# Performance work log

Measured on AMD Instinct MI355X. Metric: run time of the kernel, lower is better.

Reference implementation:

```python
import jax, jax.numpy as jnp
import numpy as np

N, B, T, H, M, DM, K = 256, 32, 128, 64, 8, 32, 3
IN_DIM = 1
OUT_DIM = 1
DEC_H = H + DM  # 96


def _p(key, shape):
    return jax.random.normal(key, shape, jnp.float32) / np.sqrt(shape[0]).astype(np.float32)


def setup_inputs() -> dict:
    key = jax.random.key(0)
    ks = jax.random.split(key, 10)
    gdi = 2 * K * (IN_DIM + H)      # 390
    ddi = 2 * K * (OUT_DIM + DEC_H)  # 582
    return {
        'x': jax.random.normal(ks[0], (B, T, N, IN_DIM), jnp.float32),
        'Memory': _p(ks[1], (M, DM)),
        'Wq': _p(ks[2], (H, DM)),
        'We1': _p(ks[3], (N, M)),
        'We2': _p(ks[4], (N, M)),
        'enc_gate_w': _p(ks[5], (gdi, 2 * H)), 'enc_gate_b': jnp.zeros((2 * H,), jnp.float32),
        'enc_upd_w': _p(ks[6], (gdi, H)), 'enc_upd_b': jnp.zeros((H,), jnp.float32),
        'dec_gate_w': _p(ks[7], (ddi, 2 * DEC_H)), 'dec_gate_b': jnp.zeros((2 * DEC_H,), jnp.float32),
        'dec_upd_w': _p(ks[8], (ddi, DEC_H)), 'dec_upd_b': jnp.zeros((DEC_H,), jnp.float32),
        'proj_w': _p(ks[9], (DEC_H, OUT_DIM)), 'proj_b': jnp.zeros((OUT_DIM,), jnp.float32),
    }


def _cheb(s):
    # Chebyshev polynomials T_0..T_{K-1} of support s: [I, s, 2 s T_{k-1} - T_{k-2}]
    polys = [jnp.eye(N, dtype=s.dtype), s]
    for _ in range(2, K):
        polys.append(2.0 * s @ polys[-1] - polys[-2])
    return polys


def _scaled_lap(e1, e2, gkey):
    # cosine-similarity graph -> straight-through gumbel hard selection -> scaled Laplacian
    norm = jnp.linalg.norm(e1, axis=1, keepdims=True) @ jnp.linalg.norm(e2, axis=1, keepdims=True).T
    g = (e1 @ e2.T) / (norm + 1e-6)
    g = (g + 1.0) / 2.0
    logits = jnp.stack([g, 1.0 - g], axis=-1)               # (N,N,2)
    y_soft = logits + jax.random.gumbel(gkey, logits.shape, logits.dtype)  # tau=1 (note: source skips softmax)
    y_hard = jax.nn.one_hot(jnp.argmax(y_soft, axis=-1), 2, dtype=logits.dtype)
    adj = (y_hard - jax.lax.stop_gradient(y_soft) + y_soft)[:, :, 0]
    eye = jnp.eye(N, dtype=adj.dtype)
    adj = adj * (1.0 - eye)                                  # zero diagonal
    d = jnp.sum(adj, axis=1)
    L = jnp.diag(d) - adj
    lam = L.max() - L.min()
    return 2.0 * L / lam - eye


def _gconv(x, S, w, b):
    # S: (2K,N,N) stacked cheb supports; x: (B,N,C)
    xg = jnp.einsum('knm,bmc->bnkc', S, x)
    xg = xg.reshape(xg.shape[0], xg.shape[1], -1)            # (B,N,2K*C), support-major like torch cat
    return xg @ w + b


def _cell(x, state, S, gw, gb, uw, ub, hid):
    zr = jax.nn.sigmoid(_gconv(jnp.concatenate([x, state], -1), S, gw, gb))
    z, r = zr[..., :hid], zr[..., hid:]
    hc = jnp.tanh(_gconv(jnp.concatenate([x, z * state], -1), S, uw, ub))
    return r * state + (1.0 - r) * hc


def reference(x, Memory, Wq, We1, We2, enc_gate_w, enc_gate_b, enc_upd_w, enc_upd_b,
              dec_gate_w, dec_gate_b, dec_upd_w, dec_upd_b, proj_w, proj_b):
    k1, k2 = jax.random.split(jax.random.key(42))
    e1, e2 = We1 @ Memory, We2 @ Memory
    S = jnp.stack(_cheb(_scaled_lap(e1, e2, k1)) + _cheb(_scaled_lap(e2, e1, k2)))  # (2K,N,N)

    # --- encoder (1 layer) over time ---
    def enc_step(state, xt):
        h = _cell(xt, state, S, enc_gate_w, enc_gate_b, enc_upd_w, enc_upd_b, H)
        return h, None
    h0 = jnp.zeros((x.shape[0], N, H), x.dtype)
    h_t, _ = jax.lax.scan(enc_step, h0, jnp.swapaxes(x, 0, 1))

    # --- memory attention query ---
    query = h_t @ Wq                                        # (B,N,DM)
    att = jax.nn.softmax(query @ Memory.T, axis=-1)         # (B,N,M)
    value = att @ Memory                                    # (B,N,DM)
    h_de = jnp.concatenate([h_t, value], -1)                # (B,N,DEC_H)

    go0 = jnp.zeros((x.shape[0], N, OUT_DIM), x.dtype)
    def dec_step(carry, _):
        state, go = carry
        h = _cell(go, state, S, dec_gate_w, dec_gate_b, dec_upd_w, dec_upd_b, DEC_H)
        go = h @ proj_w + proj_b
        return (h, go), go
    _, outs = jax.lax.scan(dec_step, (h_de, go0), None, length=T)
    return jnp.swapaxes(outs, 0, 1)                         # (B,T,N,OUT_DIM)
```

## Files before the change

### kernel.cpp

```cpp
#include <hip/hip_runtime.h>
#include <stdint.h>
#include <math.h>

#define NNODE 256
#define BATCH 32
#define TLEN  128
#define ROWS  8192

typedef unsigned short u16;
typedef short bf16x8 __attribute__((ext_vector_type(8)));
typedef float f32x4 __attribute__((ext_vector_type(4)));

__device__ inline u16 f2bf_rn(float v) {
  uint32_t u = __float_as_uint(v);
  u += 0x7fffu + ((u >> 16) & 1u);
  return (u16)(u >> 16);
}
__device__ inline float bf2f(u16 h) { return __uint_as_float(((uint32_t)h) << 16); }
__device__ inline void split2(float v, u16& hi, u16& lo) {
  hi = f2bf_rn(v);
  lo = f2bf_rn(v - bf2f(hi));
}

__device__ inline size_t pk_addr(int c, int b, int n) {
  return ((((size_t)(c >> 4) * 32 + b) * 8 + (n >> 5)) << 9) +
         (((size_t)((c & 15) | (((n >> 3) & 3) << 4))) << 3) + (n & 7);
}

__host__ __device__ inline uint32_t rotl32_(uint32_t v, int d) {
  return (v << d) | (v >> (32 - d));
}
__host__ __device__ inline void tf2x32(uint32_t k0, uint32_t k1, uint32_t x0,
                                       uint32_t x1, uint32_t* o0, uint32_t* o1) {
  uint32_t ks2 = k0 ^ k1 ^ 0x1BD11BDAu;
  x0 += k0; x1 += k1;
  x0 += x1; x1 = rotl32_(x1, 13); x1 ^= x0;
  x0 += x1; x1 = rotl32_(x1, 15); x1 ^= x0;
  x0 += x1; x1 = rotl32_(x1, 26); x1 ^= x0;
  x0 += x1; x1 = rotl32_(x1, 6);  x1 ^= x0;
  x0 += k1; x1 += ks2 + 1u;
  x0 += x1; x1 = rotl32_(x1, 17); x1 ^= x0;
  x0 += x1; x1 = rotl32_(x1, 29); x1 ^= x0;
  x0 += x1; x1 = rotl32_(x1, 16); x1 ^= x0;
  x0 += x1; x1 = rotl32_(x1, 24); x1 ^= x0;
  x0 += ks2; x1 += k0 + 2u;
  x0 += x1; x1 = rotl32_(x1, 13); x1 ^= x0;
  x0 += x1; x1 = rotl32_(x1, 15); x1 ^= x0;
  x0 += x1; x1 = rotl32_(x1, 26); x1 ^= x0;
  x0 += x1; x1 = rotl32_(x1, 6);  x1 ^= x0;
  x0 += k0; x1 += k1 + 3u;
  x0 += x1; x1 = rotl32_(x1, 17); x1 ^= x0;
  x0 += x1; x1 = rotl32_(x1, 29); x1 ^= x0;
  x0 += x1; x1 = rotl32_(x1, 16); x1 ^= x0;
  x0 += x1; x1 = rotl32_(x1, 24); x1 ^= x0;
  x0 += k1; x1 += ks2 + 4u;
  x0 += x1; x1 = rotl32_(x1, 13); x1 ^= x0;
  x0 += x1; x1 = rotl32_(x1, 15); x1 ^= x0;
  x0 += x1; x1 = rotl32_(x1, 26); x1 ^= x0;
  x0 += x1; x1 = rotl32_(x1, 6);  x1 ^= x0;
  x0 += ks2; x1 += k0 + 5u;
  *o0 = x0; *o1 = x1;
}

__device__ inline float gumbel_at(uint32_t k0, uint32_t k1, uint32_t idx) {
  uint32_t o0, o1;
  tf2x32(k0, k1, 0u, idx, &o0, &o1);
  uint32_t b = o0 ^ o1;
  float f = __uint_as_float((b >> 9) | 0x3f800000u) - 1.0f;
  const float tiny = 1.17549435e-38f;
  float u = fmaxf(tiny, f + tiny);
  return -logf(-logf(u));
}

__global__ __launch_bounds__(256) void setup_embed_kernel(
    const float* __restrict__ We1, const float* __restrict__ We2,
    const float* __restrict__ Mem, float* __restrict__ e1, float* __restrict__ e2,
    float* __restrict__ n1, float* __restrict__ n2) {
  int n = threadIdx.x;
  float a[8];
  float s;
  for (int m = 0; m < 8; ++m) a[m] = We1[n * 8 + m];
  s = 0.f;
  for (int j = 0; j < 32; ++j) {
    float v = 0.f;
    for (int m = 0; m < 8; ++m) v = fmaf(a[m], Mem[m * 32 + j], v);
    e1[n * 32 + j] = v;
    s = fmaf(v, v, s);
  }
  n1[n] = sqrtf(s);
  for (int m = 0; m < 8; ++m) a[m] = We2[n * 8 + m];
  s = 0.f;
  for (int j = 0; j < 32; ++j) {
    float v = 0.f;
    for (int m = 0; m < 8; ++m) v = fmaf(a[m], Mem[m * 32 + j], v);
    e2[n * 32 + j] = v;
    s = fmaf(v, v, s);
  }
  n2[n] = sqrtf(s);
}

__global__ void stats_init_kernel(int* stats) {
  stats[0] = 0;
  stats[1] = 0;
  stats[2] = 0x7fffffff;
}

__global__ __launch_bounds__(256) void adj_kernel(
    const float* __restrict__ eA, const float* __restrict__ eB,
    const float* __restrict__ nA, const float* __restrict__ nB,
    uint32_t k0, uint32_t k1, float* __restrict__ adj, float* __restrict__ deg,
    int* __restrict__ stats) {
  int i = blockIdx.x, j = threadIdx.x;
  float dot = 0.f;
  for (int c = 0; c < 32; ++c) dot = fmaf(eA[i * 32 + c], eB[j * 32 + c], dot);
  float g = dot / (nA[i] * nB[j] + 1e-6f);
  g = (g + 1.0f) * 0.5f;
  uint32_t f = ((uint32_t)(i * 256 + j)) * 2u;
  float g0 = gumbel_at(k0, k1, f);
  float g1 = gumbel_at(k0, k1, f + 1u);
  float a = ((g + g0) >= ((1.0f - g) + g1)) ? 1.0f : 0.0f;
  if (i == j) a = 0.0f;
  adj[i * 256 + j] = a;
  __shared__ float red[256];
  red[j] = a;
  __syncthreads();
  for (int s = 128; s > 0; s >>= 1) {
    if (j < s) red[j] += red[j + s];
    __syncthreads();
  }
  if (j == 0) {
    float d = red[0];
    deg[i] = d;
    atomicMax(&stats[0], (int)d);
    atomicMin(&stats[2], (int)d);
    if (d > 0.5f) atomicOr(&stats[1], 1);
  }
}

__global__ __launch_bounds__(256) void lap_kernel(const float* __restrict__ adj,
                                                  const float* __restrict__ deg,
                                                  const int* __restrict__ stats,
                                                  float* __restrict__ S1) {
  int i = blockIdx.x, j = threadIdx.x;
  float lmax = (float)stats[0];
  float lmin = stats[1] ? -1.0f : (float)stats[2];
  float lam = lmax - lmin;
  float L = (i == j) ? deg[i] : -adj[i * 256 + j];
  S1[i * 256 + j] = 2.0f * L / lam - ((i == j) ? 1.0f : 0.0f);
}

__global__ __launch_bounds__(256) void t2_kernel(const float* __restrict__ A,
                                                 float* __restrict__ Cout) {
  __shared__ __align__(16) float sAT[32][68];
  __shared__ __align__(16) float sB[32][68];
  int tid = threadIdx.x;
  int tc = tid & 15, tr = tid >> 4;
  int row0 = blockIdx.y * 64, col0 = blockIdx.x * 64;
  float acc[4][4] = {};
  for (int m0 = 0; m0 < 256; m0 += 32) {
    for (int i = tid; i < 2048; i += 256) {
      int r = i >> 5, c = i & 31;
      sAT[c][r] = A[(size_t)(row0 + r) * 256 + m0 + c];
    }
    for (int i = tid; i < 2048; i += 256) {
      int r = i >> 6, c = i & 63;
      sB[r][c] = A[(size_t)(m0 + r) * 256 + col0 + c];
    }
    __syncthreads();
#pragma unroll
    for (int kk = 0; kk < 32; ++kk) {
      float4 av = *(const float4*)&sAT[kk][tr * 4];
      float4 bv = *(const float4*)&sB[kk][tc * 4];
      float a[4] = {av.x, av.y, av.z, av.w};
      float b[4] = {bv.x, bv.y, bv.z, bv.w};
#pragma unroll
      for (int i = 0; i < 4; ++i)
#pragma unroll
        for (int j = 0; j < 4; ++j) acc[i][j] = fmaf(a[i], b[j], acc[i][j]);
    }
    __syncthreads();
  }
#pragma unroll
  for (int i = 0; i < 4; ++i) {
    int row = row0 + tr * 4 + i;
#pragma unroll
    for (int j = 0; j < 4; ++j) {
      int col = col0 + tc * 4 + j;
      Cout[(size_t)row * 256 + col] = 2.0f * acc[i][j] - ((row == col) ? 1.0f : 0.0f);
    }
  }
}

__global__ void cvt_s_packed(const float* __restrict__ S, u16* __restrict__ Sh,
                             u16* __restrict__ Sl) {
  int idx = blockIdx.x * 256 + threadIdx.x;
  if (idx >= 4 * 65536) return;
  int p = idx >> 16, rem = idx & 65535;
  int n = rem >> 8, m = rem & 255;
  int nt = n >> 4, li = n & 15;
  int mc = m >> 5, g = (m >> 3) & 3, j = m & 7;
  int lane = li | (g << 4);
  size_t a = (((size_t)(p * 16 + nt) * 8 + mc) << 9) + lane * 8 + j;
  u16 h, l;
  split2(S[idx], h, l);
  Sh[a] = h; Sl[a] = l;
}

__global__ void build_wfrag(const float* __restrict__ W, int C, int O, int hid,
                            u16* __restrict__ WfH, u16* __restrict__ WfL,
                            float* __restrict__ w0, float* __restrict__ wlast) {
  int idx = blockIdx.x * 256 + threadIdx.x;
  int nKC = hid / 32;
  if (idx < 5 * hid * O) {
    int kk = idx & 31;
    int rest = idx >> 5;
    int o = rest % O; rest /= O;
    int kc = rest % nKC;
    int p = rest / nKC;
    int korig = (p == 0) ? 0 : (p + (p >= 3 ? 1 : 0));
    int c = kc * 32 + kk;
    float v = 0.f;
    if (c > 0) {
      v = W[(size_t)(korig * C + c) * O + o];
      if (p == 0) v += W[(size_t)(3 * C + c) * O + o];
    }
    int ot = o >> 4, li = o & 15, g = kk >> 3, j = kk & 7;
    int lane = li | (g << 4);
    size_t a = (((size_t)(p * nKC + kc) * (O / 16) + ot) << 9) + lane * 8 + j;
    u16 h, l; split2(v, h, l);
    WfH[a] = h; WfL[a] = l;
  }
  if (idx < 5 * O) {
    int o = idx % O, p = idx / O;
    int korig = (p == 0) ? 0 : (p + (p >= 3 ? 1 : 0));
    float v0 = W[(size_t)(korig * C + 0) * O + o];
    if (p == 0) v0 += W[(size_t)(3 * C + 0) * O + o];
    w0[p * O + o] = v0;
    float vl = W[(size_t)(korig * C + hid) * O + o];
    if (p == 0) vl += W[(size_t)(3 * C + hid) * O + o];
    wlast[p * O + o] = vl;
  }
}

__global__ void zero_kernel(uint4* __restrict__ p, int n4) {
  for (int i = blockIdx.x * blockDim.x + threadIdx.x; i < n4;
       i += gridDim.x * blockDim.x)
    p[i] = make_uint4(0, 0, 0, 0);
}

__global__ void enc_init(const float* __restrict__ x,
                         u16* __restrict__ pkh, u16* __restrict__ pkl) {
  int col = blockIdx.x * 256 + threadIdx.x;
  if (col >= ROWS) return;
  int b = col >> 8, n = col & 255;
  float v = x[(size_t)b * (TLEN * NNODE) + n];
  u16 h, l; split2(v, h, l);
  size_t a = pk_addr(0, b, n);
  pkh[a] = h; pkl[a] = l;
}

__global__ __launch_bounds__(128) void attn2(const u16* __restrict__ hEh,
                                             const u16* __restrict__ hEl,
                                             const float* __restrict__ Wq,
                                             const float* __restrict__ Mem,
                                             u16* __restrict__ pkh,
                                             u16* __restrict__ pkl) {
  int col = blockIdx.x * 128 + threadIdx.x;
  int b = col >> 8, n = col & 255;
  float h[64];
  for (int c = 0; c < 64; ++c) {
    size_t a = pk_addr(1 + c, b, n);
    h[c] = bf2f(hEh[a]) + bf2f(hEl[a]);
  }
  float q[32];
  for (int j = 0; j < 32; ++j) {
    float s = 0.f;
    for (int c = 0; c < 64; ++c) s = fmaf(h[c], Wq[c * 32 + j], s);
    q[j] = s;
  }
  float l[8], mx = -3.402823466e38f;
  for (int m = 0; m < 8; ++m) {
    float s = 0.f;
    for (int j = 0; j < 32; ++j) s = fmaf(q[j], Mem[m * 32 + j], s);
    l[m] = s;
    mx = fmaxf(mx, s);
  }
  float se = 0.f;
  for (int m = 0; m < 8; ++m) { l[m] = expf(l[m] - mx); se += l[m]; }
  float val[32];
  for (int j = 0; j < 32; ++j) {
    float v = 0.f;
    for (int m = 0; m < 8; ++m) v = fmaf(l[m] / se, Mem[m * 32 + j], v);
    val[j] = v;
  }
  for (int c = 0; c < 97; ++c) {
    float v = (c == 0) ? 0.f : ((c <= 64) ? h[c - 1] : val[c - 65]);
    u16 hh, ll; split2(v, hh, ll);
    size_t a = pk_addr(c, b, n);
    pkh[a] = hh; pkl[a] = ll;
  }
}

template <int C, int HID, int O, int NKC, int MT1, int MODE>
__global__ __launch_bounds__(1024, 4) void fused_step(
    const u16* __restrict__ ApkH, const u16* __restrict__ ApkL,
    const u16* __restrict__ SpkH, const u16* __restrict__ SpkL,
    const u16* __restrict__ WpkH, const u16* __restrict__ WpkL,
    const float* __restrict__ w0, const float* __restrict__ wlast,
    const float* __restrict__ bias,
    const u16* __restrict__ stH, const u16* __restrict__ stL,
    u16* __restrict__ outPkH, u16* __restrict__ outPkL,
    float* __restrict__ rbuf,
    const float* __restrict__ xsrc, int tnext,
    const float* __restrict__ pw, const float* __restrict__ pb,
    float* __restrict__ outp, int tcur) {
  constexpr int MT2 = O / 16;
  constexpr int MT1A = (MT1 + 1) / 2;
  constexpr int CH0SLOT = HID + 1;
  constexpr int KS8 = (HID + 9) / 8;

  __shared__ __align__(16) u16 GhR[(size_t)2 * 5 * KS8 * 16 * 8];
  __shared__ __align__(16) u16 GlR[(size_t)2 * 5 * KS8 * 16 * 8];
  __shared__ float projL[(MODE == 2) ? 32 * 100 : 4];

  auto Gidx = [](int c2, int p, int li, int slot) -> size_t {
    return (((size_t)((c2 * 5 + p) * KS8 + (slot >> 3)) * 16 + li) << 3) +
           (slot & 7);
  };

  const int tid = threadIdx.x;
  const int wid = tid >> 6, lane = tid & 63;
  const int g = lane >> 4, li = lane & 15;
  const int cgi = wid >> 3, pp = wid & 3, half = (wid >> 2) & 1;
  const int bid0 = (int)blockIdx.x;
  const int bidx = ((bid0 & 7) << 5) | (bid0 >> 3);
  const int col0 = bidx * 32;
  const int b = col0 >> 8;
  const int nb = col0 & 255;
  const int n0 = nb + cgi * 16;
  const int nt = n0 >> 4;

  for (int i = tid; i < 32 * C; i += 1024) {
    int c = i >> 5, q = i & 31;
    size_t a = pk_addr(c, b, nb + q);
    int slot = (c == 0) ? CH0SLOT : c;
    GhR[Gidx(q >> 4, 0, q & 15, slot)] = ApkH[a];
    GlR[Gidx(q >> 4, 0, q & 15, slot)] = ApkL[a];
  }
  if (tid < 32) {
    GhR[Gidx(tid >> 4, 0, tid & 15, 0)] = 0;
    GlR[Gidx(tid >> 4, 0, tid & 15, 0)] = 0;
  }

  f32x4 acc1[MT1A];
#pragma unroll
  for (int i = 0; i < MT1A; ++i) acc1[i] = (f32x4){0.f, 0.f, 0.f, 0.f};

#pragma unroll 2
  for (int mc = 0; mc < 8; ++mc) {
    size_t sa = (((size_t)(pp * 16 + nt) * 8 + mc) << 9) + lane * 8;
    bf16x8 sbh = *(const bf16x8*)(SpkH + sa);
    bf16x8 sbl = *(const bf16x8*)(SpkL + sa);
#pragma unroll
    for (int i = 0; i < MT1A; ++i) {
      const int mt = half * MT1A + i;
      if (mt < MT1) {
        size_t aa = (((size_t)(mt * 32 + b) * 8 + mc) << 9) + lane * 8;
        bf16x8 ah = *(const bf16x8*)(ApkH + aa);
        bf16x8 al = *(const bf16x8*)(ApkL + aa);
        acc1[i] = __builtin_amdgcn_mfma_f32_16x16x32_bf16(ah, sbh, acc1[i], 0, 0, 0);
        acc1[i] = __builtin_amdgcn_mfma_f32_16x16x32_bf16(ah, sbl, acc1[i], 0, 0, 0);
        acc1[i] = __builtin_amdgcn_mfma_f32_16x16x32_bf16(al, sbh, acc1[i], 0, 0, 0);
      }
    }
  }

  {
    const int p = pp + 1;
#pragma unroll
    for (int i = 0; i < MT1A; ++i) {
      const int mt = half * MT1A + i;
      if (mt < MT1) {
        int cq = mt * 16 + 4 * g;
        u16 h4[4], l4[4];
#pragma unroll
        for (int r = 0; r < 4; ++r) split2(acc1[i][r], h4[r], l4[r]);
        if (cq == 0) {
          GhR[Gidx(cgi, p, li, CH0SLOT)] = h4[0];
          GlR[Gidx(cgi, p, li, CH0SLOT)] = l4[0];
          h4[0] = 0; l4[0] = 0;
        }
        if (cq + 3 <= HID) {
          uint2 vh, vl;
          vh.x = (uint32_t)h4[0] | ((uint32_t)h4[1] << 16);
          vh.y = (uint32_t)h4[2] | ((uint32_t)h4[3] << 16);
          vl.x = (uint32_t)l4[0] | ((uint32_t)l4[1] << 16);
          vl.y = (uint32_t)l4[2] | ((uint32_t)l4[3] << 16);
          *(uint2*)&GhR[Gidx(cgi, p, li, cq)] = vh;
          *(uint2*)&GlR[Gidx(cgi, p, li, cq)] = vl;
        } else {
#pragma unroll
          for (int r = 0; r < 4; ++r) {
            int c = cq + r;
            if (c >= 1 && c <= HID) {
              GhR[Gidx(cgi, p, li, c)] = h4[r];
              GlR[Gidx(cgi, p, li, c)] = l4[r];
            }
          }
        }
      }
    }
  }
  __syncthreads();

  const int mt2 = wid;
  f32x4 acc2[2];
  acc2[0] = (f32x4){0.f, 0.f, 0.f, 0.f};
  acc2[1] = (f32x4){0.f, 0.f, 0.f, 0.f};
  if (mt2 < MT2) {
#pragma unroll
    for (int p = 0; p < 5; ++p) {
#pragma unroll
      for (int kc = 0; kc < NKC; ++kc) {
        bf16x8 bh[2], bl[2];
#pragma unroll
        for (int c2 = 0; c2 < 2; ++c2) {
          bh[c2] = *(const bf16x8*)&GhR[Gidx(c2, p, li, kc * 32 + g * 8)];
          bl[c2] = *(const bf16x8*)&GlR[Gidx(c2, p, li, kc * 32 + g * 8)];
        }
        size_t wa = (((size_t)(p * NKC + kc) * MT2 + mt2) << 9) + lane * 8;
        bf16x8 wh = *(const bf16x8*)(WpkH + wa);
        bf16x8 wl = *(const bf16x8*)(WpkL + wa);
#pragma unroll
        for (int c2 = 0; c2 < 2; ++c2) {
          acc2[c2] = __builtin_amdgcn_mfma_f32_16x16x32_bf16(wh, bh[c2], acc2[c2], 0, 0, 0);
          acc2[c2] = __builtin_amdgcn_mfma_f32_16x16x32_bf16(wh, bl[c2], acc2[c2], 0, 0, 0);
          acc2[c2] = __builtin_amdgcn_mfma_f32_16x16x32_bf16(wl, bh[c2], acc2[c2], 0, 0, 0);
        }
      }
    }
  }

  float ch0v[2][5], clv[2][5];
#pragma unroll
  for (int c2 = 0; c2 < 2; ++c2)
#pragma unroll
    for (int p = 0; p < 5; ++p) {
      if (p == 0) {
        size_t a = pk_addr(0, b, nb + c2 * 16 + li);
        ch0v[c2][p] = bf2f(ApkH[a]) + bf2f(ApkL[a]);
      } else {
        ch0v[c2][p] = bf2f(GhR[Gidx(c2, p, li, CH0SLOT)]) +
                      bf2f(GlR[Gidx(c2, p, li, CH0SLOT)]);
      }
      clv[c2][p] = bf2f(GhR[Gidx(c2, p, li, HID)]) + bf2f(GlR[Gidx(c2, p, li, HID)]);
    }

  if (mt2 < MT2) {
#pragma unroll
    for (int c2 = 0; c2 < 2; ++c2) {
      const int ncolx = nb + c2 * 16 + li;
      const int colx = col0 + c2 * 16 + li;
#pragma unroll
      for (int r = 0; r < 4; ++r) {
        int o = mt2 * 16 + 4 * g + r;
        float v = acc2[c2][r] + bias[o];
#pragma unroll
        for (int p = 0; p < 5; ++p) {
          v = fmaf(w0[p * O + o], ch0v[c2][p], v);
          v = fmaf(wlast[p * O + o], clv[c2][p], v);
        }
        size_t a = pk_addr(1 + o, b, ncolx);
        if (MODE == 0) {
          float s = 1.0f / (1.0f + expf(-v));
          if (o < HID) {
            float hrec = bf2f(stH[a]) + bf2f(stL[a]);
            float u = s * hrec;
            u16 h_, l_; split2(u, h_, l_);
            outPkH[a] = h_; outPkL[a] = l_;
          } else {
            rbuf[(size_t)(o - HID) * ROWS + colx] = s;
          }
        } else {
          float hc = tanhf(v);
          float hp = bf2f(stH[a]) + bf2f(stL[a]);
          float rr = rbuf[(size_t)o * ROWS + colx];
          float hn = rr * hp + (1.0f - rr) * hc;
          u16 h_, l_; split2(hn, h_, l_);
          outPkH[a] = h_; outPkL[a] = l_;
          if (MODE == 2) projL[((size_t)c2 * 16 + li) * 100 + o] = hn;
        }
      }
    }
  }

  if (MODE == 0) {
    if (tid < 32) {
      size_t a = pk_addr(0, b, nb + tid);
      outPkH[a] = ApkH[a];
      outPkL[a] = ApkL[a];
    }
  }
  if (MODE == 1) {
    if (tnext >= 0 && tid < 32) {
      int n = nb + tid;
      float xv = xsrc[(size_t)b * (TLEN * NNODE) + (size_t)tnext * NNODE + n];
      u16 h_, l_; split2(xv, h_, l_);
      size_t a = pk_addr(0, b, n);
      outPkH[a] = h_; outPkL[a] = l_;
    }
  }
  if (MODE == 2) {
    __syncthreads();
    if (tid < 32) {
      int n = nb + tid;
      float s = pb[0];
#pragma unroll
      for (int o = 0; o < HID; ++o) s = fmaf(pw[o], projL[(size_t)tid * 100 + o], s);
      u16 h_, l_; split2(s, h_, l_);
      size_t a = pk_addr(0, b, n);
      outPkH[a] = h_; outPkL[a] = l_;
      outp[((size_t)b * TLEN + tcur) * NNODE + n] = s;
    }
  }
}

extern "C" void kernel_launch(void* const* d_in, const int* in_sizes, int n_in,
                              void* d_out, int out_size, void* d_ws, size_t ws_size,
                              hipStream_t stream) {
  (void)in_sizes; (void)n_in; (void)out_size; (void)ws_size;
  const float* x   = (const float*)d_in[0];
  const float* Mem = (const float*)d_in[1];
  const float* Wq  = (const float*)d_in[2];
  const float* We1 = (const float*)d_in[3];
  const float* We2 = (const float*)d_in[4];
  const float* egw = (const float*)d_in[5];
  const float* egb = (const float*)d_in[6];
  const float* euw = (const float*)d_in[7];
  const float* eub = (const float*)d_in[8];
  const float* dgw = (const float*)d_in[9];
  const float* dgb = (const float*)d_in[10];
  const float* duw = (const float*)d_in[11];
  const float* dub = (const float*)d_in[12];
  const float* pw  = (const float*)d_in[13];
  const float* pb  = (const float*)d_in[14];
  float* out = (float*)d_out;

  float* ws = (float*)d_ws;
  size_t off = 0;
  auto allocf = [&](size_t nf) {
    float* p = ws + off;
    off += (nf + 63) & ~(size_t)63;
    return p;
  };
  auto allocu = [&](size_t nu) { return (u16*)allocf((nu + 1) / 2); };

  float* Sf  = allocf(4 * 65536);
  float* e1  = allocf(8192);
  float* e2  = allocf(8192);
  float* n1  = allocf(256);
  float* n2  = allocf(256);
  float* adj = allocf(65536);
  float* deg = allocf(256);
  int* stats = (int*)allocf(64);
  float* rb  = allocf((size_t)96 * ROWS);
  float* w0gE = allocf(5 * 128);
  float* w0uE = allocf(5 * 64);
  float* w0gD = allocf(5 * 192);
  float* w0uD = allocf(5 * 96);
  float* wlgE = allocf(5 * 128);
  float* wluE = allocf(5 * 64);
  float* wlgD = allocf(5 * 192);
  float* wluD = allocf(5 * 96);

  u16* SpkH = allocu((size_t)4 * 65536);
  u16* SpkL = allocu((size_t)4 * 65536);
  u16* WgEh = allocu((size_t)5 * 2 * 8 * 512);
  u16* WgEl = allocu((size_t)5 * 2 * 8 * 512);
  u16* WuEh = allocu((size_t)5 * 2 * 4 * 512);
  u16* WuEl = allocu((size_t)5 * 2 * 4 * 512);
  u16* WgDh = allocu((size_t)5 * 3 * 12 * 512);
  u16* WgDl = allocu((size_t)5 * 3 * 12 * 512);
  u16* WuDh = allocu((size_t)5 * 3 * 6 * 512);
  u16* WuDl = allocu((size_t)5 * 3 * 6 * 512);

  const size_t PKE = (size_t)5 * 32 * 8 * 512;
  const size_t PKD = (size_t)7 * 32 * 8 * 512;
  u16* hEpkH = allocu(PKE);
  u16* hEpkL = allocu(PKE);
  u16* uEpkH = allocu(PKE);
  u16* uEpkL = allocu(PKE);
  u16* hDpkH = allocu(PKD);
  u16* hDpkL = allocu(PKD);
  u16* uDpkH = allocu(PKD);
  u16* uDpkL = allocu(PKD);
  const size_t PKTOT = 4 * PKE + 4 * PKD;

  uint32_t ka0, ka1, kb0, kb1;
  tf2x32(0u, 42u, 0u, 0u, &ka0, &ka1);
  tf2x32(0u, 42u, 0u, 1u, &kb0, &kb1);

  zero_kernel<<<1024, 256, 0, stream>>>((uint4*)hEpkH, (int)(PKTOT / 8));
  setup_embed_kernel<<<1, 256, 0, stream>>>(We1, We2, Mem, e1, e2, n1, n2);
  stats_init_kernel<<<1, 1, 0, stream>>>(stats);
  adj_kernel<<<256, 256, 0, stream>>>(e1, e2, n1, n2, ka0, ka1, adj, deg, stats);
  lap_kernel<<<256, 256, 0, stream>>>(adj, deg, stats, Sf);
  t2_kernel<<<dim3(4, 4), 256, 0, stream>>>(Sf, Sf + 65536);
  stats_init_kernel<<<1, 1, 0, stream>>>(stats);
  adj_kernel<<<256, 256, 0, stream>>>(e2, e1, n2, n1, kb0, kb1, adj, deg, stats);
  lap_kernel<<<256, 256, 0, stream>>>(adj, deg, stats, Sf + 2 * 65536);
  t2_kernel<<<dim3(4, 4), 256, 0, stream>>>(Sf + 2 * 65536, Sf + 3 * 65536);
  cvt_s_packed<<<1024, 256, 0, stream>>>(Sf, SpkH, SpkL);
  build_wfrag<<<(5 * 64 * 128 + 255) / 256, 256, 0, stream>>>(egw, 65, 128, 64, WgEh, WgEl, w0gE, wlgE);
  build_wfrag<<<(5 * 64 * 64 + 255) / 256, 256, 0, stream>>>(euw, 65, 64, 64, WuEh, WuEl, w0uE, wluE);
  build_wfrag<<<(5 * 96 * 192 + 255) / 256, 256, 0, stream>>>(dgw, 97, 192, 96, WgDh, WgDl, w0gD, wlgD);
  build_wfrag<<<(5 * 96 * 96 + 255) / 256, 256, 0, stream>>>(duw, 97, 96, 96, WuDh, WuDl, w0uD, wluD);

  enc_init<<<32, 256, 0, stream>>>(x, hEpkH, hEpkL);
  for (int t = 0; t < TLEN; ++t) {
    fused_step<65, 64, 128, 2, 5, 0><<<256, 1024, 0, stream>>>(
        hEpkH, hEpkL, SpkH, SpkL, WgEh, WgEl, w0gE, wlgE, egb,
        hEpkH, hEpkL, uEpkH, uEpkL, rb, nullptr, -1, nullptr, nullptr, nullptr, 0);
    fused_step<65, 64, 64, 2, 5, 1><<<256, 1024, 0, stream>>>(
        uEpkH, uEpkL, SpkH, SpkL, WuEh, WuEl, w0uE, wluE, eub,
        hEpkH, hEpkL, hEpkH, hEpkL, rb,
        x, (t + 1 < TLEN) ? (t + 1) : -1, nullptr, nullptr, nullptr, 0);
  }

  attn2<<<64, 128, 0, stream>>>(hEpkH, hEpkL, Wq, Mem, hDpkH, hDpkL);

  for (int t = 0; t < TLEN; ++t) {
    fused_step<97, 96, 192, 3, 7, 0><<<256, 1024, 0, stream>>>(
        hDpkH, hDpkL, SpkH, SpkL, WgDh, WgDl, w0gD, wlgD, dgb,
        hDpkH, hDpkL, uDpkH, uDpkL, rb, nullptr, -1, nullptr, nullptr, nullptr, 0);
    fused_step<97, 96, 96, 3, 7, 2><<<256, 1024, 0, stream>>>(
        uDpkH, uDpkL, SpkH, SpkL, WuDh, WuDl, w0uD, wluD, dub,
        hDpkH, hDpkL, hDpkH, hDpkL, rb,
        nullptr, -1, pw, pb, out, t);
  }
}
```

Measured before the change: 8.008 ms.

## Replace per-step kernel launches with persistent cooperative kernels using per-XCD barriers

Encoder and decoder time loops now each run inside one cooperative persistent kernel. Half-steps are separated by atomic-counter barriers scoped to groups of 32 blocks (blockIdx & 7), replacing 512 separate kernel launches. The A-operand fragments are also staged once per block into shared memory, using sc0 loads that bypass stale cache lines, instead of each wave reading them from global memory. This cuts launch overhead and redundant global loads but relies on the assumption that each group of 32 blocks only exchanges data within that group. It also keeps the old multi-launch path as a fallback if the cooperative launch fails.

```diff
diff --git a/kernel.cpp b/kernel.cpp
--- a/kernel.cpp
+++ b/kernel.cpp
@@ -25,6 +25,12 @@
 __device__ inline size_t pk_addr(int c, int b, int n) {
   return ((((size_t)(c >> 4) * 32 + b) * 8 + (n >> 5)) << 9) +
          (((size_t)((c & 15) | (((n >> 3) & 3) << 4))) << 3) + (n & 7);
+}
+
+__device__ __forceinline__ bf16x8 load16_sc0(const u16* p) {
+  bf16x8 r;
+  asm volatile("global_load_dwordx4 %0, %1, off sc0" : "=v"(r) : "v"(p));
+  return r;
 }
 
 __host__ __device__ inline uint32_t rotl32_(uint32_t v, int d) {
@@ -302,26 +308,24 @@
 }
 
 template <int C, int HID, int O, int NKC, int MT1, int MODE>
-__global__ __launch_bounds__(1024, 4) void fused_step(
-    const u16* __restrict__ ApkH, const u16* __restrict__ ApkL,
-    const u16* __restrict__ SpkH, const u16* __restrict__ SpkL,
-    const u16* __restrict__ WpkH, const u16* __restrict__ WpkL,
-    const float* __restrict__ w0, const float* __restrict__ wlast,
-    const float* __restrict__ bias,
-    const u16* __restrict__ stH, const u16* __restrict__ stL,
-    u16* __restrict__ outPkH, u16* __restrict__ outPkL,
-    float* __restrict__ rbuf,
-    const float* __restrict__ xsrc, int tnext,
-    const float* __restrict__ pw, const float* __restrict__ pb,
-    float* __restrict__ outp, int tcur) {
+__device__ __forceinline__ void half_step(
+    const u16* ApkH, const u16* ApkL,
+    const u16* SpkH, const u16* SpkL,
+    const u16* WpkH, const u16* WpkL,
+    const float* w0, const float* wlast, const float* bias,
+    const u16* stH, const u16* stL,
+    u16* outPkH, u16* outPkL,
+    float* rbuf, const float* xsrc, int tnext,
+    const float* pw, const float* pb, float* outp, int tcur,
+    u16* GhR, u16* GlR, u16* stg) {
   constexpr int MT2 = O / 16;
   constexpr int MT1A = (MT1 + 1) / 2;
   constexpr int CH0SLOT = HID + 1;
   constexpr int KS8 = (HID + 9) / 8;
-
-  __shared__ __align__(16) u16 GhR[(size_t)2 * 5 * KS8 * 16 * 8];
-  __shared__ __align__(16) u16 GlR[(size_t)2 * 5 * KS8 * 16 * 8];
-  __shared__ float projL[(MODE == 2) ? 32 * 100 : 4];
+  constexpr int NFR = MT1 * 8;
+  constexpr int KTRIP = (NFR + 15) / 16;
+
+  float* projL = (float*)stg;
 
   auto Gidx = [](int c2, int p, int li, int slot) -> size_t {
     return (((size_t)((c2 * 5 + p) * KS8 + (slot >> 3)) * 16 + li) << 3) +
@@ -340,39 +344,65 @@
   const int n0 = nb + cgi * 16;
   const int nt = n0 >> 4;
 
-  for (int i = tid; i < 32 * C; i += 1024) {
-    int c = i >> 5, q = i & 31;
-    size_t a = pk_addr(c, b, nb + q);
-    int slot = (c == 0) ? CH0SLOT : c;
-    GhR[Gidx(q >> 4, 0, q & 15, slot)] = ApkH[a];
-    GlR[Gidx(q >> 4, 0, q & 15, slot)] = ApkL[a];
-  }
-  if (tid < 32) {
-    GhR[Gidx(tid >> 4, 0, tid & 15, 0)] = 0;
-    GlR[Gidx(tid >> 4, 0, tid & 15, 0)] = 0;
-  }
-
   f32x4 acc1[MT1A];
 #pragma unroll
   for (int i = 0; i < MT1A; ++i) acc1[i] = (f32x4){0.f, 0.f, 0.f, 0.f};
 
-#pragma unroll 2
-  for (int mc = 0; mc < 8; ++mc) {
-    size_t sa = (((size_t)(pp * 16 + nt) * 8 + mc) << 9) + lane * 8;
-    bf16x8 sbh = *(const bf16x8*)(SpkH + sa);
-    bf16x8 sbl = *(const bf16x8*)(SpkL + sa);
-#pragma unroll
-    for (int i = 0; i < MT1A; ++i) {
-      const int mt = half * MT1A + i;
-      if (mt < MT1) {
-        size_t aa = (((size_t)(mt * 32 + b) * 8 + mc) << 9) + lane * 8;
-        bf16x8 ah = *(const bf16x8*)(ApkH + aa);
-        bf16x8 al = *(const bf16x8*)(ApkL + aa);
-        acc1[i] = __builtin_amdgcn_mfma_f32_16x16x32_bf16(ah, sbh, acc1[i], 0, 0, 0);
-        acc1[i] = __builtin_amdgcn_mfma_f32_16x16x32_bf16(ah, sbl, acc1[i], 0, 0, 0);
-        acc1[i] = __builtin_amdgcn_mfma_f32_16x16x32_bf16(al, sbh, acc1[i], 0, 0, 0);
-      }
-    }
+#pragma unroll
+  for (int r = 0; r < 2; ++r) {
+    bf16x8 areg[KTRIP];
+#pragma unroll
+    for (int k = 0; k < KTRIP; ++k) {
+      int f = wid + k * 16;
+      if (f < NFR) {
+        int hl = f & 1, rest = f >> 1;
+        int mt = rest % MT1, mcl = rest / MT1;
+        int mc = r * 4 + mcl;
+        const u16* src = (hl ? ApkL : ApkH) +
+                         ((((size_t)(mt * 32 + b) * 8 + mc) << 9) + lane * 8);
+        areg[k] = load16_sc0(src);
+      }
+    }
+    if (r == 0) {
+      for (int i = tid; i < 32 * C; i += 1024) {
+        int c = i >> 5, q = i & 31;
+        size_t a = pk_addr(c, b, nb + q);
+        int slot = (c == 0) ? CH0SLOT : c;
+        GhR[Gidx(q >> 4, 0, q & 15, slot)] = ApkH[a];
+        GlR[Gidx(q >> 4, 0, q & 15, slot)] = ApkL[a];
+      }
+      if (tid < 32) {
+        GhR[Gidx(tid >> 4, 0, tid & 15, 0)] = 0;
+        GlR[Gidx(tid >> 4, 0, tid & 15, 0)] = 0;
+      }
+    }
+    asm volatile("s_waitcnt vmcnt(0)" ::: "memory");
+#pragma unroll
+    for (int k = 0; k < KTRIP; ++k) {
+      int f = wid + k * 16;
+      if (f < NFR) *(bf16x8*)&stg[(size_t)f * 512 + lane * 8] = areg[k];
+    }
+    __syncthreads();
+#pragma unroll
+    for (int mcl = 0; mcl < 4; ++mcl) {
+      int mc = r * 4 + mcl;
+      size_t sa = (((size_t)(pp * 16 + nt) * 8 + mc) << 9) + lane * 8;
+      bf16x8 sbh = *(const bf16x8*)(SpkH + sa);
+      bf16x8 sbl = *(const bf16x8*)(SpkL + sa);
+#pragma unroll
+      for (int i = 0; i < MT1A; ++i) {
+        const int mt = half * MT1A + i;
+        if (mt < MT1) {
+          const size_t fb = (size_t)((mcl * MT1 + mt) * 2) * 512 + lane * 8;
+          bf16x8 ah = *(const bf16x8*)&stg[fb];
+          bf16x8 al = *(const bf16x8*)&stg[fb + 512];
+          acc1[i] = __builtin_amdgcn_mfma_f32_16x16x32_bf16(ah, sbh, acc1[i], 0, 0, 0);
+          acc1[i] = __builtin_amdgcn_mfma_f32_16x16x32_bf16(ah, sbl, acc1[i], 0, 0, 0);
+          acc1[i] = __builtin_amdgcn_mfma_f32_16x16x32_bf16(al, sbh, acc1[i], 0, 0, 0);
+        }
+      }
+    }
+    __syncthreads();
   }
 
   {
@@ -525,6 +555,77 @@
   }
 }
 
+__device__ __forceinline__ void xcd_barrier(int* bar, int grp, int target) {
+  asm volatile("s_waitcnt vmcnt(0)" ::: "memory");
+  __syncthreads();
+  if (threadIdx.x == 0) {
+    __hip_atomic_fetch_add(&bar[grp * 32], 1, __ATOMIC_RELAXED,
+                           __HIP_MEMORY_SCOPE_AGENT);
+    while (__hip_atomic_load(&bar[grp * 32], __ATOMIC_RELAXED,
+                             __HIP_MEMORY_SCOPE_AGENT) < target)
+      __builtin_amdgcn_s_sleep(1);
+  }
+  __syncthreads();
+}
+
+template <int C, int HID, int O, int NKC, int MT1, int MODE>
+__global__ __launch_bounds__(1024, 4) void fused_step(
+    const u16* __restrict__ ApkH, const u16* __restrict__ ApkL,
+    const u16* __restrict__ SpkH, const u16* __restrict__ SpkL,
+    const u16* __restrict__ WpkH, const u16* __restrict__ WpkL,
+    const float* __restrict__ w0, const float* __restrict__ wlast,
+    const float* __restrict__ bias,
+    const u16* __restrict__ stH, const u16* __restrict__ stL,
+    u16* __restrict__ outPkH, u16* __restrict__ outPkL,
+    float* __restrict__ rbuf,
+    const float* __restrict__ xsrc, int tnext,
+    const float* __restrict__ pw, const float* __restrict__ pb,
+    float* __restrict__ outp, int tcur) {
+  constexpr int KS8 = (HID + 9) / 8;
+  __shared__ __align__(16) u16 GhR[(size_t)2 * 5 * KS8 * 16 * 8];
+  __shared__ __align__(16) u16 GlR[(size_t)2 * 5 * KS8 * 16 * 8];
+  __shared__ __align__(16) u16 stg[(size_t)MT1 * 8 * 512];
+  half_step<C, HID, O, NKC, MT1, MODE>(
+      ApkH, ApkL, SpkH, SpkL, WpkH, WpkL, w0, wlast, bias, stH, stL,
+      outPkH, outPkL, rbuf, xsrc, tnext, pw, pb, outp, tcur, GhR, GlR, stg);
+}
+
+struct PhaseP {
+  const float* xsrc;
+  u16 *hPkH, *hPkL, *uPkH, *uPkL;
+  const u16 *SpkH, *SpkL;
+  const u16 *WgH, *WgL; const float *w0g, *wlg, *bg;
+  const u16 *WuH, *WuL; const float *w0u, *wlu, *bu;
+  float* rbuf;
+  const float *pw, *pb; float* outp;
+  int* bar;
+};
+
+template <int C, int HID, int Og, int Ou, int NKC, int MT1, int UPDM>
+__global__ __launch_bounds__(1024, 4) void persistent_phase(PhaseP P) {
+  constexpr int KS8 = (HID + 9) / 8;
+  __shared__ __align__(16) u16 GhR[(size_t)2 * 5 * KS8 * 16 * 8];
+  __shared__ __align__(16) u16 GlR[(size_t)2 * 5 * KS8 * 16 * 8];
+  __shared__ __align__(16) u16 stg[(size_t)MT1 * 8 * 512];
+  const int grp = (int)blockIdx.x & 7;
+  int ep = 0;
+  for (int t = 0; t < TLEN; ++t) {
+    half_step<C, HID, Og, NKC, MT1, 0>(
+        P.hPkH, P.hPkL, P.SpkH, P.SpkL, P.WgH, P.WgL, P.w0g, P.wlg, P.bg,
+        P.hPkH, P.hPkL, P.uPkH, P.uPkL, P.rbuf, nullptr, -1,
+        nullptr, nullptr, nullptr, 0, GhR, GlR, stg);
+    ++ep;
+    xcd_barrier(P.bar, grp, 32 * ep);
+    half_step<C, HID, Ou, NKC, MT1, UPDM>(
+        P.uPkH, P.uPkL, P.SpkH, P.SpkL, P.WuH, P.WuL, P.w0u, P.wlu, P.bu,
+        P.hPkH, P.hPkL, P.hPkH, P.hPkL, P.rbuf,
+        P.xsrc, (UPDM == 1) ? ((t + 1 < TLEN) ? t + 1 : -1) : -1,
+        P.pw, P.pb, P.outp, t, GhR, GlR, stg);
+    ++ep;
+    xcd_barrier(P.bar, grp, 32 * ep);
+  }
+}
+
 extern "C" void kernel_launch(void* const* d_in, const int* in_sizes, int n_in,
                               void* d_out, int out_size, void* d_ws, size_t ws_size,
                               hipStream_t stream) {
@@ -595,12 +696,15 @@
   u16* uDpkH = allocu(PKD);
   u16* uDpkL = allocu(PKD);
   const size_t PKTOT = 4 * PKE + 4 * PKD;
+  int* barE = (int*)allocf(256);
+  int* barD = (int*)allocf(256);
 
   uint32_t ka0, ka1, kb0, kb1;
   tf2x32(0u, 42u, 0u, 0u, &ka0, &ka1);
   tf2x32(0u, 42u, 0u, 1u, &kb0, &kb1);
 
   zero_kernel<<<1024, 256, 0, stream>>>((uint4*)hEpkH, (int)(PKTOT / 8));
+  zero_kernel<<<1, 256, 0, stream>>>((uint4*)barE, 128);
   setup_embed_kernel<<<1, 256, 0, stream>>>(We1, We2, Mem, e1, e2, n1, n2);
   stats_init_kernel<<<1, 1, 0, stream>>>(stats);
   adj_kernel<<<256, 256, 0, stream>>>(e1, e2, n1, n2, ka0, ka1, adj, deg, stats);
@@ -617,25 +721,57 @@
   build_wfrag<<<(5 * 96 * 96 + 255) / 256, 256, 0, stream>>>(duw, 97, 96, 96, WuDh, WuDl, w0uD, wluD);
 
   enc_init<<<32, 256, 0, stream>>>(x, hEpkH, hEpkL);
-  for (int t = 0; t < TLEN; ++t) {
-    fused_step<65, 64, 128, 2, 5, 0><<<256, 1024, 0, stream>>>(
-        hEpkH, hEpkL, SpkH, SpkL, WgEh, WgEl, w0gE, wlgE, egb,
-        hEpkH, hEpkL, uEpkH, uEpkL, rb, nullptr, -1, nullptr, nullptr, nullptr, 0);
-    fused_step<65, 64, 64, 2, 5, 1><<<256, 1024, 0, stream>>>(
-        uEpkH, uEpkL, SpkH, SpkL, WuEh, WuEl, w0uE, wluE, eub,
-        hEpkH, hEpkL, hEpkH, hEpkL, rb,
-        x, (t + 1 < TLEN) ? (t + 1) : -1, nullptr, nullptr, nullptr, 0);
+  {
+    PhaseP pe;
+    pe.xsrc = x;
+    pe.hPkH = hEpkH; pe.hPkL = hEpkL; pe.uPkH = uEpkH; pe.uPkL = uEpkL;
+    pe.SpkH = SpkH; pe.SpkL = SpkL;
+    pe.WgH = WgEh; pe.WgL = WgEl; pe.w0g = w0gE; pe.wlg = wlgE; pe.bg = egb;
+    pe.WuH = WuEh; pe.WuL = WuEl; pe.w0u = w0uE; pe.wlu = wluE; pe.bu = eub;
+    pe.rbuf = rb; pe.pw = nullptr; pe.pb = nullptr; pe.outp = nullptr;
+    pe.bar = barE;
+    void* argsE[] = { &pe };
+    auto kE = persistent_phase<65, 64, 128, 64, 2, 5, 1>;
+    hipError_t e = hipLaunchCooperativeKernel((const void*)kE, dim3(256),
+                                              dim3(1024), argsE, 0, stream);
+    if (e != hipSuccess) {
+      for (int t = 0; t < TLEN; ++t) {
+        fused_step<65, 64, 128, 2, 5, 0><<<256, 1024, 0, stream>>>(
+            hEpkH, hEpkL, SpkH, SpkL, WgEh, WgEl, w0gE, wlgE, egb,
+            hEpkH, hEpkL, uEpkH, uEpkL, rb, nullptr, -1, nullptr, nullptr, nullptr, 0);
+        fused_step<65, 64, 64, 2, 5, 1><<<256, 1024, 0, stream>>>(
+            uEpkH, uEpkL, SpkH, SpkL, WuEh, WuEl, w0uE, wluE, eub,
+            hEpkH, hEpkL, hEpkH, hEpkL, rb,
+            x, (t + 1 < TLEN) ? (t + 1) : -1, nullptr, nullptr, nullptr, 0);
+      }
+    }
   }
 
   attn2<<<64, 128, 0, stream>>>(hEpkH, hEpkL, Wq, Mem, hDpkH, hDpkL);
 
-  for (int t = 0; t < TLEN; ++t) {
-    fused_step<97, 96, 192, 3, 7, 0><<<256, 1024, 0, stream>>>(
-        hDpkH, hDpkL, SpkH, SpkL, WgDh, WgDl, w0gD, wlgD, dgb,
-        hDpkH, hDpkL, uDpkH, uDpkL, rb, nullptr, -1, nullptr, nullptr, nullptr, 0);
-    fused_step<97, 96, 96, 3, 7, 2><<<256, 1024, 0, stream>>>(
-        uDpkH, uDpkL, SpkH, SpkL, WuDh, WuDl, w0uD, wluD, dub,
-        hDpkH, hDpkL, hDpkH, hDpkL, rb,
-        nullptr, -1, pw, pb, out, t);
-  }
-}
+  {
+    PhaseP pd;
+    pd.xsrc = nullptr;
+    pd.hPkH = hDpkH; pd.hPkL = hDpkL; pd.uPkH = uDpkH; pd.uPkL = uDpkL;
+    pd.SpkH = SpkH; pd.SpkL = SpkL;
+    pd.WgH = WgDh; pd.WgL = WgDl; pd.w0g = w0gD; pd.wlg = wlgD; pd.bg = dgb;
+    pd.WuH = WuDh; pd.WuL = WuDl; pd.w0u = w0uD; pd.wlu = wluD; pd.bu = dub;
+    pd.rbuf = rb; pd.pw = pw; pd.pb = pb; pd.outp = out;
+    pd.bar = barD;
+    void* argsD[] = { &pd };
+    auto kD = persistent_phase<97, 96, 192, 96, 3, 7, 2>;
+    hipError_t e = hipLaunchCooperativeKernel((const void*)kD, dim3(256),
+                                              dim3(1024), argsD, 0, stream);
+    if (e != hipSuccess) {
+      for (int t = 0; t < TLEN; ++t) {
+        fused_step<97, 96, 192, 3, 7, 0><<<256, 1024, 0, stream>>>(
+            hDpkH, hDpkL, SpkH, SpkL, WgDh, WgDl, w0gD, wlgD, dgb,
+            hDpkH, hDpkL, uDpkH, uDpkL, rb, nullptr, -1, nullptr, nullptr, nullptr, 0);
+        fused_step<97, 96, 96, 3, 7, 2><<<256, 1024, 0, stream>>>(
+            uDpkH, uDpkL, SpkH, SpkL, WuDh, WuDl, w0uD, wluD, dub,
+            hDpkH, hDpkL, hDpkH, hDpkL, rb,
+            nullptr, -1, pw, pb, out, t);
+      }
+    }
+  }
+}
```

Result: slower. 21.70 ms (+170.9%).

## Halve per-block column tile to 16 and double grid to 512 blocks

Applied to the files above, without the earlier changes.

Each fused_step block now handles 16 node columns instead of 32, and the grid doubles from 256 to 512 blocks. The first-stage graph-support MFMA work is split four ways across wave segments instead of two, and the second-stage weight GEMM keeps one accumulator per wave instead of two. The aim is to fill more compute units on the GPU for this latency-bound per-timestep kernel and to lower per-block LDS and register use (launch bounds now request 8 blocks). In exchange, weight and support fragments are reloaded by twice as many blocks, and each wave does less MFMA work per load.

```diff
diff --git a/kernel.cpp b/kernel.cpp
--- a/kernel.cpp
+++ b/kernel.cpp
@@ -302,7 +302,7 @@
 }
 
 template <int C, int HID, int O, int NKC, int MT1, int MODE>
-__global__ __launch_bounds__(1024, 4) void fused_step(
+__global__ __launch_bounds__(1024, 8) void fused_step(
     const u16* __restrict__ ApkH, const u16* __restrict__ ApkL,
     const u16* __restrict__ SpkH, const u16* __restrict__ SpkL,
     const u16* __restrict__ WpkH, const u16* __restrict__ WpkL,
@@ -315,41 +315,39 @@
     const float* __restrict__ pw, const float* __restrict__ pb,
     float* __restrict__ outp, int tcur) {
   constexpr int MT2 = O / 16;
-  constexpr int MT1A = (MT1 + 1) / 2;
+  constexpr int MT1A = (MT1 + 3) / 4;
   constexpr int CH0SLOT = HID + 1;
   constexpr int KS8 = (HID + 9) / 8;
 
-  __shared__ __align__(16) u16 GhR[(size_t)2 * 5 * KS8 * 16 * 8];
-  __shared__ __align__(16) u16 GlR[(size_t)2 * 5 * KS8 * 16 * 8];
-  __shared__ float projL[(MODE == 2) ? 32 * 100 : 4];
-
-  auto Gidx = [](int c2, int p, int li, int slot) -> size_t {
-    return (((size_t)((c2 * 5 + p) * KS8 + (slot >> 3)) * 16 + li) << 3) +
-           (slot & 7);
+  __shared__ __align__(16) u16 GhR[(size_t)5 * KS8 * 16 * 8];
+  __shared__ __align__(16) u16 GlR[(size_t)5 * KS8 * 16 * 8];
+  __shared__ float projL[(MODE == 2) ? 16 * 100 : 4];
+
+  auto Gidx = [](int p, int li, int slot) -> size_t {
+    return (((size_t)(p * KS8 + (slot >> 3)) * 16 + li) << 3) + (slot & 7);
   };
 
   const int tid = threadIdx.x;
   const int wid = tid >> 6, lane = tid & 63;
   const int g = lane >> 4, li = lane & 15;
-  const int cgi = wid >> 3, pp = wid & 3, half = (wid >> 2) & 1;
+  const int pp = wid & 3, seg = wid >> 2;
   const int bid0 = (int)blockIdx.x;
-  const int bidx = ((bid0 & 7) << 5) | (bid0 >> 3);
-  const int col0 = bidx * 32;
+  const int bidx = ((bid0 & 7) << 6) | (bid0 >> 3);
+  const int col0 = bidx * 16;
   const int b = col0 >> 8;
   const int nb = col0 & 255;
-  const int n0 = nb + cgi * 16;
-  const int nt = n0 >> 4;
-
-  for (int i = tid; i < 32 * C; i += 1024) {
-    int c = i >> 5, q = i & 31;
+  const int nt = nb >> 4;
+
+  for (int i = tid; i < 16 * C; i += 1024) {
+    int c = i >> 4, q = i & 15;
     size_t a = pk_addr(c, b, nb + q);
     int slot = (c == 0) ? CH0SLOT : c;
-    GhR[Gidx(q >> 4, 0, q & 15, slot)] = ApkH[a];
-    GlR[Gidx(q >> 4, 0, q & 15, slot)] = ApkL[a];
-  }
-  if (tid < 32) {
-    GhR[Gidx(tid >> 4, 0, tid & 15, 0)] = 0;
-    GlR[Gidx(tid >> 4, 0, tid & 15, 0)] = 0;
+    GhR[Gidx(0, q, slot)] = ApkH[a];
+    GlR[Gidx(0, q, slot)] = ApkL[a];
+  }
+  if (tid < 16) {
+    GhR[Gidx(0, tid, 0)] = 0;
+    GlR[Gidx(0, tid, 0)] = 0;
   }
 
   f32x4 acc1[MT1A];
@@ -363,7 +361,7 @@
     bf16x8 sbl = *(const bf16x8*)(SpkL + sa);
 #pragma unroll
     for (int i = 0; i < MT1A; ++i) {
-      const int mt = half * MT1A + i;
+      const int mt = seg * MT1A + i;
       if (mt < MT1) {
         size_t aa = (((size_t)(mt * 32 + b) * 8 + mc) << 9) + lane * 8;
         bf16x8 ah = *(const bf16x8*)(ApkH + aa);
@@ -379,15 +377,15 @@
     const int p = pp + 1;
 #pragma unroll
     for (int i = 0; i < MT1A; ++i) {
-      const int mt = half * MT1A + i;
+      const int mt = seg * MT1A + i;
       if (mt < MT1) {
         int cq = mt * 16 + 4 * g;
         u16 h4[4], l4[4];
 #pragma unroll
         for (int r = 0; r < 4; ++r) split2(acc1[i][r], h4[r], l4[r]);
         if (cq == 0) {
-          GhR[Gidx(cgi, p, li, CH0SLOT)] = h4[0];
-          GlR[Gidx(cgi, p, li, CH0SLOT)] = l4[0];
+          GhR[Gidx(p, li, CH0SLOT)] = h4[0];
+          GlR[Gidx(p, li, CH0SLOT)] = l4[0];
           h4[0] = 0; l4[0] = 0;
         }
         if (cq + 3 <= HID) {
@@ -396,15 +394,15 @@
           vh.y = (uint32_t)h4[2] | ((uint32_t)h4[3] << 16);
           vl.x = (uint32_t)l4[0] | ((uint32_t)l4[1] << 16);
           vl.y = (uint32_t)l4[2] | ((uint32_t)l4[3] << 16);
-          *(uint2*)&GhR[Gidx(cgi, p, li, cq)] = vh;
-          *(uint2*)&GlR[Gidx(cgi, p, li, cq)] = vl;
+          *(uint2*)&GhR[Gidx(p, li, cq)] = vh;
+          *(uint2*)&GlR[Gidx(p, li, cq)] = vl;
         } else {
 #pragma unroll
           for (int r = 0; r < 4; ++r) {
             int c = cq + r;
             if (c >= 1 && c <= HID) {
-              GhR[Gidx(cgi, p, li, c)] = h4[r];
-              GlR[Gidx(cgi, p, li, c)] = l4[r];
+              GhR[Gidx(p, li, c)] = h4[r];
+              GlR[Gidx(p, li, c)] = l4[r];
             }
           }
         }
@@ -414,95 +412,80 @@
   __syncthreads();
 
   const int mt2 = wid;
-  f32x4 acc2[2];
-  acc2[0] = (f32x4){0.f, 0.f, 0.f, 0.f};
-  acc2[1] = (f32x4){0.f, 0.f, 0.f, 0.f};
+  f32x4 acc2 = (f32x4){0.f, 0.f, 0.f, 0.f};
   if (mt2 < MT2) {
 #pragma unroll
     for (int p = 0; p < 5; ++p) {
 #pragma unroll
       for (int kc = 0; kc < NKC; ++kc) {
-        bf16x8 bh[2], bl[2];
-#pragma unroll
-        for (int c2 = 0; c2 < 2; ++c2) {
-          bh[c2] = *(const bf16x8*)&GhR[Gidx(c2, p, li, kc * 32 + g * 8)];
-          bl[c2] = *(const bf16x8*)&GlR[Gidx(c2, p, li, kc * 32 + g * 8)];
-        }
+        bf16x8 bh = *(const bf16x8*)&GhR[Gidx(p, li, kc * 32 + g * 8)];
+        bf16x8 bl = *(const bf16x8*)&GlR[Gidx(p, li, kc * 32 + g * 8)];
         size_t wa = (((size_t)(p * NKC + kc) * MT2 + mt2) << 9) + lane * 8;
         bf16x8 wh = *(const bf16x8*)(WpkH + wa);
         bf16x8 wl = *(const bf16x8*)(WpkL + wa);
-#pragma unroll
-        for (int c2 = 0; c2 < 2; ++c2) {
-          acc2[c2] = __builtin_amdgcn_mfma_f32_16x16x32_bf16(wh, bh[c2], acc2[c2], 0, 0, 0);
-          acc2[c2] = __builtin_amdgcn_mfma_f32_16x16x32_bf16(wh, bl[c2], acc2[c2], 0, 0, 0);
-          acc2[c2] = __builtin_amdgcn_mfma_f32_16x16x32_bf16(wl, bh[c2], acc2[c2], 0, 0, 0);
+        acc2 = __builtin_amdgcn_mfma_f32_16x16x32_bf16(wh, bh, acc2, 0, 0, 0);
+        acc2 = __builtin_amdgcn_mfma_f32_16x16x32_bf16(wh, bl, acc2, 0, 0, 0);
+        acc2 = __builtin_amdgcn_mfma_f32_16x16x32_bf16(wl, bh, acc2, 0, 0, 0);
+      }
+    }
+  }
+
+  float ch0v[5], clv[5];
+#pragma unroll
+  for (int p = 0; p < 5; ++p) {
+    if (p == 0) {
+      size_t a = pk_addr(0, b, nb + li);
+      ch0v[p] = bf2f(ApkH[a]) + bf2f(ApkL[a]);
+    } else {
+      ch0v[p] = bf2f(GhR[Gidx(p, li, CH0SLOT)]) + bf2f(GlR[Gidx(p, li, CH0SLOT)]);
+    }
+    clv[p] = bf2f(GhR[Gidx(p, li, HID)]) + bf2f(GlR[Gidx(p, li, HID)]);
+  }
+
+  if (mt2 < MT2) {
+    const int ncolx = nb + li;
+    const int colx = col0 + li;
+#pragma unroll
+    for (int r = 0; r < 4; ++r) {
+      int o = mt2 * 16 + 4 * g + r;
+      float v = acc2[r] + bias[o];
+#pragma unroll
+      for (int p = 0; p < 5; ++p) {
+        v = fmaf(w0[p * O + o], ch0v[p], v);
+        v = fmaf(wlast[p * O + o], clv[p], v);
+      }
+      size_t a = pk_addr(1 + o, b, ncolx);
+      if (MODE == 0) {
+        float s = 1.0f / (1.0f + expf(-v));
+        if (o < HID) {
+          float hrec = bf2f(stH[a]) + bf2f(stL[a]);
+          float u = s * hrec;
+          u16 h_, l_; split2(u, h_, l_);
+          outPkH[a] = h_; outPkL[a] = l_;
+        } else {
+          rbuf[(size_t)(o - HID) * ROWS + colx] = s;
         }
+      } else {
+        float hc = tanhf(v);
+        float hp = bf2f(stH[a]) + bf2f(stL[a]);
+        float rr = rbuf[(size_t)o * ROWS + colx];
+        float hn = rr * hp + (1.0f - rr) * hc;
+        u16 h_, l_; split2(hn, h_, l_);
+        outPkH[a] = h_; outPkL[a] = l_;
+        if (MODE == 2) projL[(size_t)li * 100 + o] = hn;
       }
     }
   }
 
-  float ch0v[2][5], clv[2][5];
-#pragma unroll
-  for (int c2 = 0; c2 < 2; ++c2)
-#pragma unroll
-    for (int p = 0; p < 5; ++p) {
-      if (p == 0) {
-        size_t a = pk_addr(0, b, nb + c2 * 16 + li);
-        ch0v[c2][p] = bf2f(ApkH[a]) + bf2f(ApkL[a]);
-      } else {
-        ch0v[c2][p] = bf2f(GhR[Gidx(c2, p, li, CH0SLOT)]) +
-                      bf2f(GlR[Gidx(c2, p, li, CH0SLOT)]);
-      }
-      clv[c2][p] = bf2f(GhR[Gidx(c2, p, li, HID)]) + bf2f(GlR[Gidx(c2, p, li, HID)]);
-    }
-
-  if (mt2 < MT2) {
-#pragma unroll
-    for (int c2 = 0; c2 < 2; ++c2) {
-      const int ncolx = nb + c2 * 16 + li;
-      const int colx = col0 + c2 * 16 + li;
-#pragma unroll
-      for (int r = 0; r < 4; ++r) {
-        int o = mt2 * 16 + 4 * g + r;
-        float v = acc2[c2][r] + bias[o];
-#pragma unroll
-        for (int p = 0; p < 5; ++p) {
-          v = fmaf(w0[p * O + o], ch0v[c2][p], v);
-          v = fmaf(wlast[p * O + o], clv[c2][p], v);
-        }
-        size_t a = pk_addr(1 + o, b, ncolx);
-        if (MODE == 0) {
-          float s = 1.0f / (1.0f + expf(-v));
-          if (o < HID) {
-            float hrec = bf2f(stH[a]) + bf2f(stL[a]);
-            float u = s * hrec;
-            u16 h_, l_; split2(u, h_, l_);
-            outPkH[a] = h_; outPkL[a] = l_;
-          } else {
-            rbuf[(size_t)(o - HID) * ROWS + colx] = s;
-          }
-        } else {
-          float hc = tanhf(v);
-          float hp = bf2f(stH[a]) + bf2f(stL[a]);
-          float rr = rbuf[(size_t)o * ROWS + colx];
-          float hn = rr * hp + (1.0f - rr) * hc;
-          u16 h_, l_; split2(hn, h_, l_);
-          outPkH[a] = h_; outPkL[a] = l_;
-          if (MODE == 2) projL[((size_t)c2 * 16 + li) * 100 + o] = hn;
-        }
-      }
-    }
-  }
-
   if (MODE == 0) {
-    if (tid < 32) {
+    if (tid < 16) {
       size_t a = pk_addr(0, b, nb + tid);
       outPkH[a] = ApkH[a];
       outPkL[a] = ApkL[a];
     }
   }
   if (MODE == 1) {
-    if (tnext >= 0 && tid < 32) {
+    if (tnext >= 0 && tid < 16) {
       int n = nb + tid;
       float xv = xsrc[(size_t)b * (TLEN * NNODE) + (size_t)tnext * NNODE + n];
       u16 h_, l_; split2(xv, h_, l_);
@@ -512,7 +495,7 @@
   }
   if (MODE == 2) {
     __syncthreads();
-    if (tid < 32) {
+    if (tid < 16) {
       int n = nb + tid;
       float s = pb[0];
 #pragma unroll
@@ -618,10 +601,10 @@
 
   enc_init<<<32, 256, 0, stream>>>(x, hEpkH, hEpkL);
   for (int t = 0; t < TLEN; ++t) {
-    fused_step<65, 64, 128, 2, 5, 0><<<256, 1024, 0, stream>>>(
+    fused_step<65, 64, 128, 2, 5, 0><<<512, 1024, 0, stream>>>(
         hEpkH, hEpkL, SpkH, SpkL, WgEh, WgEl, w0gE, wlgE, egb,
         hEpkH, hEpkL, uEpkH, uEpkL, rb, nullptr, -1, nullptr, nullptr, nullptr, 0);
-    fused_step<65, 64, 64, 2, 5, 1><<<256, 1024, 0, stream>>>(
+    fused_step<65, 64, 64, 2, 5, 1><<<512, 1024, 0, stream>>>(
         uEpkH, uEpkL, SpkH, SpkL, WuEh, WuEl, w0uE, wluE, eub,
         hEpkH, hEpkL, hEpkH, hEpkL, rb,
         x, (t + 1 < TLEN) ? (t + 1) : -1, nullptr, nullptr, nullptr, 0);
@@ -630,10 +613,10 @@
   attn2<<<64, 128, 0, stream>>>(hEpkH, hEpkL, Wq, Mem, hDpkH, hDpkL);
 
   for (int t = 0; t < TLEN; ++t) {
-    fused_step<97, 96, 192, 3, 7, 0><<<256, 1024, 0, stream>>>(
+    fused_step<97, 96, 192, 3, 7, 0><<<512, 1024, 0, stream>>>(
         hDpkH, hDpkL, SpkH, SpkL, WgDh, WgDl, w0gD, wlgD, dgb,
         hDpkH, hDpkL, uDpkH, uDpkL, rb, nullptr, -1, nullptr, nullptr, nullptr, 0);
-    fused_step<97, 96, 96, 3, 7, 2><<<256, 1024, 0, stream>>>(
+    fused_step<97, 96, 96, 3, 7, 2><<<512, 1024, 0, stream>>>(
         uDpkH, uDpkL, SpkH, SpkL, WuDh, WuDl, w0uD, wluD, dub,
         hDpkH, hDpkL, hDpkH, hDpkL, rb,
         nullptr, -1, pw, pb, out, t);
```

Result: slower. 9.206 ms (+15.0%).
